# Optimization experiments

Measured on AMD Instinct MI355X. Metric: run time of the kernel, lower is better.

The kernel has to match this reference:

```python
import jax, jax.numpy as jnp
import numpy as np

B, S, D, H = 4, 2048, 1024, 16
DK = D // H

def setup_inputs() -> dict:
    key = jax.random.key(0)
    ks = jax.random.split(key, 5)
    x = jax.random.normal(ks[0], (B, S, D), dtype=jnp.float32)
    scale = 1.0 / np.sqrt(D)
    Wq = jax.random.normal(ks[1], (D, D), dtype=jnp.float32) * scale
    Wk = jax.random.normal(ks[2], (D, D), dtype=jnp.float32) * scale
    Wv = jax.random.normal(ks[3], (D, D), dtype=jnp.float32) * scale
    Wo = jax.random.normal(ks[4], (D, D), dtype=jnp.float32) * scale
    return {"x": x, "Wq": Wq, "Wk": Wk, "Wv": Wv, "Wo": Wo}

def reference(x, Wq, Wk, Wv, Wo):
    # F.linear: y = x @ W.T  (weights stored torch-style [out, in])
    q = jnp.einsum('bsd,ed->bse', x, Wq).reshape(B, S, H, DK).transpose(0, 2, 1, 3)
    k = jnp.einsum('bsd,ed->bse', x, Wk).reshape(B, S, H, DK).transpose(0, 2, 1, 3)
    v = jnp.einsum('bsd,ed->bse', x, Wv).reshape(B, S, H, DK).transpose(0, 2, 1, 3)
    scores = jnp.einsum('bhqd,bhkd->bhqk', q, k) / jnp.sqrt(jnp.float32(DK))
    attn = jax.nn.softmax(scores, axis=-1)  # dropout p=0.0 -> identity
    out = jnp.einsum('bhqk,bhkd->bhqd', attn, v)
    out = out.transpose(0, 2, 1, 3).reshape(B, S, D)
    return jnp.einsum('bsd,ed->bse', out, Wo)
```

## Files before the change

kernel.cpp:

```cpp
#include <hip/hip_runtime.h>
#include <hip/hip_bf16.h>

#define B_ 4
#define S_ 2048
#define D_ 1024
#define H_ 16
#define DK_ 64

typedef __attribute__((ext_vector_type(8))) short short8;
typedef __attribute__((ext_vector_type(4))) float floatx4;
typedef __attribute__((ext_vector_type(16))) float floatx16;
typedef __attribute__((ext_vector_type(4))) unsigned int uint4v;

#define QSCL 0.1803368801111204f

static __device__ __forceinline__ unsigned short f2bf(float f) {
    unsigned int u = __float_as_uint(f);
    u += 0x7fffu + ((u >> 16) & 1u);
    return (unsigned short)(u >> 16);
}

static __device__ __forceinline__ unsigned int pack2bf_perm(float a, float b) {
    unsigned int u0 = __float_as_uint(a) + 0x8000u;
    unsigned int u1 = __float_as_uint(b) + 0x8000u;
    return __builtin_amdgcn_perm(u1, u0, 0x07060302u);
}

static __device__ __forceinline__ unsigned int pack2bf(float a, float b) {
    return (unsigned int)f2bf(a) | ((unsigned int)f2bf(b) << 16);
}

#define PLSWAP(a, b) asm volatile("v_permlane32_swap_b32 %0, %1" : "+v"(a), "+v"(b))

struct CastAll {
    const float* x;
    const float* w[4];
    unsigned short* xd;
    unsigned short* wd[4];
};

__global__ void cast_all_kernel(CastAll a) {
    int i = blockIdx.x * blockDim.x + threadIdx.x;
    const float* s;
    unsigned short* d;
    int j;
    if (i < 2097152) {
        s = a.x; d = a.xd; j = i;
    } else {
        int k = i - 2097152;
        int w = k >> 18;
        j = k & 262143;
        s = a.w[w]; d = a.wd[w];
    }
    float4 v = ((const float4*)s)[j];
    ushort4 o;
    o.x = f2bf(v.x); o.y = f2bf(v.y); o.z = f2bf(v.z); o.w = f2bf(v.w);
    ((ushort4*)d)[j] = o;
}

template <typename OutT, bool VT2>
__global__ __launch_bounds__(256) void gemm_bt(
    const unsigned short* __restrict__ A,
    const unsigned short* __restrict__ W0,
    const unsigned short* __restrict__ W1,
    const unsigned short* __restrict__ W2,
    OutT* __restrict__ C0, OutT* __restrict__ C1, OutT* __restrict__ C2,
    int M, int N, int K)
{
    __shared__ __align__(16) unsigned short At[128 * 64];
    __shared__ __align__(16) unsigned short Bt[128 * 64];

    const unsigned short* W = (blockIdx.z == 0) ? W0 : ((blockIdx.z == 1) ? W1 : W2);
    OutT* C = (blockIdx.z == 0) ? C0 : ((blockIdx.z == 1) ? C1 : C2);

    const int n0 = blockIdx.x * 128;
    const int m0 = blockIdx.y * 128;
    const int wv = threadIdx.x >> 6;
    const int ln = threadIdx.x & 63;
    const int l31 = ln & 31;
    const int half = ln >> 5;
    const int wm = (wv >> 1) * 64;
    const int wn = (wv & 1) * 64;

    floatx16 acc[2][2];
#pragma unroll
    for (int mt = 0; mt < 2; mt++)
#pragma unroll
        for (int nt = 0; nt < 2; nt++)
#pragma unroll
            for (int e = 0; e < 16; e++) acc[mt][nt][e] = 0.f;

    const int lr = ln >> 3;
    const int lc = (((ln & 7) ^ lr) * 8);
    const int sw = (l31 & 7);

    for (int k0 = 0; k0 < K; k0 += 64) {
        __syncthreads();
#pragma unroll
        for (int c = 0; c < 4; c++) {
            int rowA = wv * 32 + c * 8;
            const unsigned short* gA = A + (size_t)(m0 + rowA + lr) * K + k0 + lc;
            __builtin_amdgcn_global_load_lds(
                (const __attribute__((address_space(1))) void*)gA,
                (__attribute__((address_space(3))) void*)&At[rowA * 64], 16, 0, 0);
            const unsigned short* gB = W + (size_t)(n0 + rowA + lr) * K + k0 + lc;
            __builtin_amdgcn_global_load_lds(
                (const __attribute__((address_space(1))) void*)gB,
                (__attribute__((address_space(3))) void*)&Bt[rowA * 64], 16, 0, 0);
        }
        __syncthreads();

#pragma unroll
        for (int ks = 0; ks < 4; ks++) {
            const int slot = ((ks * 2 + half) ^ sw) * 8;
            short8 af[2], bf[2];
#pragma unroll
            for (int mt = 0; mt < 2; mt++)
                af[mt] = *(const short8*)&At[(wm + mt * 32 + l31) * 64 + slot];
#pragma unroll
            for (int nt = 0; nt < 2; nt++)
                bf[nt] = *(const short8*)&Bt[(wn + nt * 32 + l31) * 64 + slot];
#pragma unroll
            for (int mt = 0; mt < 2; mt++)
#pragma unroll
                for (int nt = 0; nt < 2; nt++)
                    acc[mt][nt] = __builtin_amdgcn_mfma_f32_32x32x16_bf16(af[mt], bf[nt], acc[mt][nt], 0, 0, 0);
        }
    }

    const float esc = (VT2 && blockIdx.z == 0) ? QSCL : 1.0f;

    if constexpr (VT2) {
        if (blockIdx.z == 2) {
            unsigned short* Vt = (unsigned short*)C;
#pragma unroll
            for (int mt = 0; mt < 2; mt++)
#pragma unroll
                for (int nt = 0; nt < 2; nt++)
#pragma unroll
                    for (int rg = 0; rg < 4; rg++) {
                        int col = n0 + wn + nt * 32 + l31;
                        int row0 = m0 + wm + mt * 32 + 4 * half + 8 * rg;
                        int bb = row0 >> 11, ss = row0 & 2047;
                        size_t addr = ((size_t)(bb * 1024 + col)) * 2048 + ss;
                        uint2 pk;
                        pk.x = pack2bf(acc[mt][nt][4 * rg + 0], acc[mt][nt][4 * rg + 1]);
                        pk.y = pack2bf(acc[mt][nt][4 * rg + 2], acc[mt][nt][4 * rg + 3]);
                        *(uint2*)(Vt + addr) = pk;
                    }
            return;
        }
    }

#pragma unroll
    for (int mt = 0; mt < 2; mt++)
#pragma unroll
        for (int nt = 0; nt < 2; nt++)
#pragma unroll
            for (int rg = 0; rg < 4; rg++)
#pragma unroll
                for (int r = 0; r < 4; r++) {
                    int row = m0 + wm + mt * 32 + 4 * half + 8 * rg + r;
                    int col = n0 + wn + nt * 32 + l31;
                    float v = acc[mt][nt][4 * rg + r] * esc;
                    if constexpr (sizeof(OutT) == 2)
                        C[(size_t)row * N + col] = (OutT)f2bf(v);
                    else
                        C[(size_t)row * N + col] = v;
                }
}

__global__ __launch_bounds__(256, 4) void flash_attn(
    const unsigned short* __restrict__ Q,
    const unsigned short* __restrict__ K,
    const unsigned short* __restrict__ Vt,
    unsigned short* __restrict__ O)
{
    __shared__ __align__(16) unsigned short Kt[64 * 72];
    __shared__ __align__(16) unsigned short VT[64 * 72];

    const int qt = blockIdx.x;
    const int h = blockIdx.y;
    const int b = blockIdx.z;
    const int tid = threadIdx.x;
    const int wv = tid >> 6;
    const int ln = tid & 63;
    const int l31 = ln & 31;
    const int half = ln >> 5;

    const size_t base = ((size_t)b * S_) * D_ + (size_t)h * DK_;
    const size_t vtbase = ((size_t)(b * 1024 + h * 64)) * (size_t)S_;

    const int qrow = qt * 128 + wv * 32 + l31;
    short8 qf[4];
    {
        const unsigned short* qp = Q + base + (size_t)qrow * D_ + half * 8;
#pragma unroll
        for (int ks = 0; ks < 4; ks++) qf[ks] = *(const short8*)(qp + ks * 16);
    }

    short8 ones;
#pragma unroll
    for (int e = 0; e < 8; e++) ones[e] = (short)0x3F80;

    floatx16 Oacc[2], lacc;
#pragma unroll
    for (int mt = 0; mt < 2; mt++)
#pragma unroll
        for (int e = 0; e < 16; e++) Oacc[mt][e] = 0.f;
#pragma unroll
    for (int e = 0; e < 16; e++) lacc[e] = 0.f;

    const int srow = tid >> 3;
    const int scol = (tid & 7) * 8;

    for (int kt = 0; kt < S_ / 64; kt++) {
        __syncthreads();
#pragma unroll
        for (int c = 0; c < 2; c++) {
            int row = srow + c * 32;
            *(short8*)&Kt[row * 72 + scol] =
                *(const short8*)(K + base + (size_t)(kt * 64 + row) * D_ + scol);
            *(short8*)&VT[row * 72 + scol] =
                *(const short8*)(Vt + vtbase + (size_t)row * S_ + kt * 64 + scol);
        }
        __syncthreads();

        floatx16 sac[2];
#pragma unroll
        for (int mt = 0; mt < 2; mt++) {
#pragma unroll
            for (int e = 0; e < 16; e++) sac[mt][e] = 0.f;
#pragma unroll
            for (int ks = 0; ks < 4; ks++) {
                short8 kf = *(const short8*)&Kt[(mt * 32 + l31) * 72 + ks * 16 + half * 8];
                sac[mt] = __builtin_amdgcn_mfma_f32_32x32x16_bf16(kf, qf[ks], sac[mt], 0, 0, 0);
            }
        }

        uint2 run[2][4];
#pragma unroll
        for (int mt = 0; mt < 2; mt++)
#pragma unroll
            for (int g = 0; g < 4; g++) {
                float p0 = __builtin_amdgcn_exp2f(sac[mt][4 * g + 0]);
                float p1 = __builtin_amdgcn_exp2f(sac[mt][4 * g + 1]);
                float p2 = __builtin_amdgcn_exp2f(sac[mt][4 * g + 2]);
                float p3 = __builtin_amdgcn_exp2f(sac[mt][4 * g + 3]);
                run[mt][g].x = pack2bf_perm(p0, p1);
                run[mt][g].y = pack2bf_perm(p2, p3);
            }

#pragma unroll
        for (int mt = 0; mt < 2; mt++)
#pragma unroll
            for (int t = 0; t < 2; t++) {
                PLSWAP(run[mt][2 * t].x, run[mt][2 * t + 1].x);
                PLSWAP(run[mt][2 * t].y, run[mt][2 * t + 1].y);
            }

#pragma unroll
        for (int mt2 = 0; mt2 < 2; mt2++)
#pragma unroll
            for (int t = 0; t < 2; t++) {
                int ks = mt2 * 2 + t;
                uint4v u = {run[mt2][2 * t].x, run[mt2][2 * t].y,
                            run[mt2][2 * t + 1].x, run[mt2][2 * t + 1].y};
                short8 pf = __builtin_bit_cast(short8, u);
#pragma unroll
                for (int mt = 0; mt < 2; mt++) {
                    short8 vf = *(const short8*)&VT[(mt * 32 + l31) * 72 + ks * 16 + half * 8];
                    Oacc[mt] = __builtin_amdgcn_mfma_f32_32x32x16_bf16(vf, pf, Oacc[mt], 0, 0, 0);
                }
                lacc = __builtin_amdgcn_mfma_f32_32x32x16_bf16(ones, pf, lacc, 0, 0, 0);
            }
    }

    float inv = 1.0f / lacc[0];

#pragma unroll
    for (int mt = 0; mt < 2; mt++)
#pragma unroll
        for (int g = 0; g < 4; g++) {
            uint2 pk;
            pk.x = pack2bf(Oacc[mt][4 * g + 0] * inv, Oacc[mt][4 * g + 1] * inv);
            pk.y = pack2bf(Oacc[mt][4 * g + 2] * inv, Oacc[mt][4 * g + 3] * inv);
            *(uint2*)(O + base + (size_t)qrow * D_ + mt * 32 + 8 * g + 4 * half) = pk;
        }
}

extern "C" void kernel_launch(void* const* d_in, const int* in_sizes, int n_in,
                              void* d_out, int out_size, void* d_ws, size_t ws_size,
                              hipStream_t stream) {
    const float* x  = (const float*)d_in[0];
    const float* Wq = (const float*)d_in[1];
    const float* Wk = (const float*)d_in[2];
    const float* Wv = (const float*)d_in[3];
    const float* Wo = (const float*)d_in[4];
    float* out = (float*)d_out;

    char* ws = (char*)d_ws;
    const size_t MB = 1024 * 1024;
    unsigned short* xb  = (unsigned short*)(ws);
    unsigned short* wqb = (unsigned short*)(ws + 16 * MB);
    unsigned short* wkb = (unsigned short*)(ws + 18 * MB);
    unsigned short* wvb = (unsigned short*)(ws + 20 * MB);
    unsigned short* wob = (unsigned short*)(ws + 22 * MB);
    unsigned short* Qb  = (unsigned short*)(ws + 24 * MB);
    unsigned short* Kb  = (unsigned short*)(ws + 40 * MB);
    unsigned short* Vtb = (unsigned short*)(ws + 56 * MB);
    unsigned short* Ob  = (unsigned short*)(ws);

    CastAll ca;
    ca.x = x; ca.xd = xb;
    ca.w[0] = Wq; ca.w[1] = Wk; ca.w[2] = Wv; ca.w[3] = Wo;
    ca.wd[0] = wqb; ca.wd[1] = wkb; ca.wd[2] = wvb; ca.wd[3] = wob;
    cast_all_kernel<<<12288, 256, 0, stream>>>(ca);

    dim3 gq(D_ / 128, (B_ * S_) / 128, 3);
    gemm_bt<unsigned short, true><<<gq, 256, 0, stream>>>(
        xb, wqb, wkb, wvb, Qb, Kb, Vtb, B_ * S_, D_, D_);

    dim3 gf(S_ / 128, H_, B_);
    flash_attn<<<gf, 256, 0, stream>>>(Qb, Kb, Vtb, Ob);

    dim3 go(D_ / 128, (B_ * S_) / 128, 1);
    gemm_bt<float, false><<<go, 256, 0, stream>>>(
        Ob, wob, wob, wob, out, out, out, B_ * S_, D_, D_);
}
```

Baseline: 287.4 us.

## Process two query subtiles per wave in flash attention to reuse K/V tiles

Each wave now handles 64 query rows (two 32-row subtiles) instead of 32, so each block covers 256 queries and every K/V tile staged in shared memory feeds twice the MFMA work. The row-sum MFMA against a ones vector is replaced by scalar accumulation of the exp values plus a cross-half shuffle at the end. Pointer increments replace the per-iteration address recomputation. The grid is halved and launch bounds are lowered to 2 blocks per CU to fit the doubled accumulator registers, at the cost of fewer blocks and less occupancy.

```diff
diff --git a/kernel.cpp b/kernel.cpp
--- a/kernel.cpp
+++ b/kernel.cpp
@@ -170,7 +170,7 @@
                 }
 }
 
-__global__ __launch_bounds__(256, 4) void flash_attn(
+__global__ __launch_bounds__(256, 2) void flash_attn(
     const unsigned short* __restrict__ Q,
     const unsigned short* __restrict__ K,
     const unsigned short* __restrict__ Vt,
@@ -191,102 +191,116 @@
     const size_t base = ((size_t)b * S_) * D_ + (size_t)h * DK_;
     const size_t vtbase = ((size_t)(b * 1024 + h * 64)) * (size_t)S_;
 
-    const int qrow = qt * 128 + wv * 32 + l31;
-    short8 qf[4];
-    {
-        const unsigned short* qp = Q + base + (size_t)qrow * D_ + half * 8;
-#pragma unroll
-        for (int ks = 0; ks < 4; ks++) qf[ks] = *(const short8*)(qp + ks * 16);
-    }
-
-    short8 ones;
-#pragma unroll
-    for (int e = 0; e < 8; e++) ones[e] = (short)0x3F80;
-
-    floatx16 Oacc[2], lacc;
-#pragma unroll
-    for (int mt = 0; mt < 2; mt++)
-#pragma unroll
-        for (int e = 0; e < 16; e++) Oacc[mt][e] = 0.f;
-#pragma unroll
-    for (int e = 0; e < 16; e++) lacc[e] = 0.f;
+    const int qrow0 = qt * 256 + wv * 64 + l31;
+    short8 qf[2][4];
+#pragma unroll
+    for (int qh = 0; qh < 2; qh++) {
+        const unsigned short* qp = Q + base + (size_t)(qrow0 + qh * 32) * D_ + half * 8;
+#pragma unroll
+        for (int ks = 0; ks < 4; ks++) qf[qh][ks] = *(const short8*)(qp + ks * 16);
+    }
+
+    floatx16 Oacc[2][2];
+#pragma unroll
+    for (int qh = 0; qh < 2; qh++)
+#pragma unroll
+        for (int mt = 0; mt < 2; mt++)
+#pragma unroll
+            for (int e = 0; e < 16; e++) Oacc[qh][mt][e] = 0.f;
+    float l_i[2] = {0.f, 0.f};
 
     const int srow = tid >> 3;
     const int scol = (tid & 7) * 8;
+    const unsigned short* kp0 = K + base + (size_t)srow * D_ + scol;
+    const unsigned short* kp1 = kp0 + (size_t)32 * D_;
+    const unsigned short* vp0 = Vt + vtbase + (size_t)srow * S_ + scol;
+    const unsigned short* vp1 = vp0 + (size_t)32 * S_;
 
     for (int kt = 0; kt < S_ / 64; kt++) {
         __syncthreads();
-#pragma unroll
-        for (int c = 0; c < 2; c++) {
-            int row = srow + c * 32;
-            *(short8*)&Kt[row * 72 + scol] =
-                *(const short8*)(K + base + (size_t)(kt * 64 + row) * D_ + scol);
-            *(short8*)&VT[row * 72 + scol] =
-                *(const short8*)(Vt + vtbase + (size_t)row * S_ + kt * 64 + scol);
-        }
+        *(short8*)&Kt[srow * 72 + scol] = *(const short8*)kp0;
+        *(short8*)&Kt[(srow + 32) * 72 + scol] = *(const short8*)kp1;
+        *(short8*)&VT[srow * 72 + scol] = *(const short8*)vp0;
+        *(short8*)&VT[(srow + 32) * 72 + scol] = *(const short8*)vp1;
+        kp0 += (size_t)64 * D_; kp1 += (size_t)64 * D_;
+        vp0 += 64; vp1 += 64;
         __syncthreads();
 
-        floatx16 sac[2];
+        uint2 run[2][2][4];
+
 #pragma unroll
         for (int mt = 0; mt < 2; mt++) {
-#pragma unroll
-            for (int e = 0; e < 16; e++) sac[mt][e] = 0.f;
+            floatx16 sac[2];
+#pragma unroll
+            for (int qh = 0; qh < 2; qh++)
+#pragma unroll
+                for (int e = 0; e < 16; e++) sac[qh][e] = 0.f;
 #pragma unroll
             for (int ks = 0; ks < 4; ks++) {
                 short8 kf = *(const short8*)&Kt[(mt * 32 + l31) * 72 + ks * 16 + half * 8];
-                sac[mt] = __builtin_amdgcn_mfma_f32_32x32x16_bf16(kf, qf[ks], sac[mt], 0, 0, 0);
+                sac[0] = __builtin_amdgcn_mfma_f32_32x32x16_bf16(kf, qf[0][ks], sac[0], 0, 0, 0);
+                sac[1] = __builtin_amdgcn_mfma_f32_32x32x16_bf16(kf, qf[1][ks], sac[1], 0, 0, 0);
             }
+#pragma unroll
+            for (int qh = 0; qh < 2; qh++)
+#pragma unroll
+                for (int g = 0; g < 4; g++) {
+                    float p0 = __builtin_amdgcn_exp2f(sac[qh][4 * g + 0]);
+                    float p1 = __builtin_amdgcn_exp2f(sac[qh][4 * g + 1]);
+                    float p2 = __builtin_amdgcn_exp2f(sac[qh][4 * g + 2]);
+                    float p3 = __builtin_amdgcn_exp2f(sac[qh][4 * g + 3]);
+                    l_i[qh] += (p0 + p1) + (p2 + p3);
+                    run[qh][mt][g].x = pack2bf_perm(p0, p1);
+                    run[qh][mt][g].y = pack2bf_perm(p2, p3);
+                }
         }
 
-        uint2 run[2][4];
-#pragma unroll
-        for (int mt = 0; mt < 2; mt++)
-#pragma unroll
-            for (int g = 0; g < 4; g++) {
-                float p0 = __builtin_amdgcn_exp2f(sac[mt][4 * g + 0]);
-                float p1 = __builtin_amdgcn_exp2f(sac[mt][4 * g + 1]);
-                float p2 = __builtin_amdgcn_exp2f(sac[mt][4 * g + 2]);
-                float p3 = __builtin_amdgcn_exp2f(sac[mt][4 * g + 3]);
-                run[mt][g].x = pack2bf_perm(p0, p1);
-                run[mt][g].y = pack2bf_perm(p2, p3);
-            }
-
-#pragma unroll
-        for (int mt = 0; mt < 2; mt++)
-#pragma unroll
-            for (int t = 0; t < 2; t++) {
-                PLSWAP(run[mt][2 * t].x, run[mt][2 * t + 1].x);
-                PLSWAP(run[mt][2 * t].y, run[mt][2 * t + 1].y);
-            }
+#pragma unroll
+        for (int qh = 0; qh < 2; qh++)
+#pragma unroll
+            for (int mt = 0; mt < 2; mt++)
+#pragma unroll
+                for (int t = 0; t < 2; t++) {
+                    PLSWAP(run[qh][mt][2 * t].x, run[qh][mt][2 * t + 1].x);
+                    PLSWAP(run[qh][mt][2 * t].y, run[qh][mt][2 * t + 1].y);
+                }
 
 #pragma unroll
         for (int mt2 = 0; mt2 < 2; mt2++)
 #pragma unroll
             for (int t = 0; t < 2; t++) {
                 int ks = mt2 * 2 + t;
-                uint4v u = {run[mt2][2 * t].x, run[mt2][2 * t].y,
-                            run[mt2][2 * t + 1].x, run[mt2][2 * t + 1].y};
-                short8 pf = __builtin_bit_cast(short8, u);
+                short8 pf[2];
+#pragma unroll
+                for (int qh = 0; qh < 2; qh++) {
+                    uint4v u = {run[qh][mt2][2 * t].x, run[qh][mt2][2 * t].y,
+                                run[qh][mt2][2 * t + 1].x, run[qh][mt2][2 * t + 1].y};
+                    pf[qh] = __builtin_bit_cast(short8, u);
+                }
 #pragma unroll
                 for (int mt = 0; mt < 2; mt++) {
                     short8 vf = *(const short8*)&VT[(mt * 32 + l31) * 72 + ks * 16 + half * 8];
-                    Oacc[mt] = __builtin_amdgcn_mfma_f32_32x32x16_bf16(vf, pf, Oacc[mt], 0, 0, 0);
-                }
-                lacc = __builtin_amdgcn_mfma_f32_32x32x16_bf16(ones, pf, lacc, 0, 0, 0);
+                    Oacc[0][mt] = __builtin_amdgcn_mfma_f32_32x32x16_bf16(vf, pf[0], Oacc[0][mt], 0, 0, 0);
+                    Oacc[1][mt] = __builtin_amdgcn_mfma_f32_32x32x16_bf16(vf, pf[1], Oacc[1][mt], 0, 0, 0);
+                }
             }
     }
 
-    float inv = 1.0f / lacc[0];
-
-#pragma unroll
-    for (int mt = 0; mt < 2; mt++)
-#pragma unroll
-        for (int g = 0; g < 4; g++) {
-            uint2 pk;
-            pk.x = pack2bf(Oacc[mt][4 * g + 0] * inv, Oacc[mt][4 * g + 1] * inv);
-            pk.y = pack2bf(Oacc[mt][4 * g + 2] * inv, Oacc[mt][4 * g + 3] * inv);
-            *(uint2*)(O + base + (size_t)qrow * D_ + mt * 32 + 8 * g + 4 * half) = pk;
-        }
+#pragma unroll
+    for (int qh = 0; qh < 2; qh++) {
+        float ls = l_i[qh] + __shfl_xor(l_i[qh], 32);
+        float inv = 1.0f / ls;
+        const size_t orow = base + (size_t)(qrow0 + qh * 32) * D_;
+#pragma unroll
+        for (int mt = 0; mt < 2; mt++)
+#pragma unroll
+            for (int g = 0; g < 4; g++) {
+                uint2 pk;
+                pk.x = pack2bf(Oacc[qh][mt][4 * g + 0] * inv, Oacc[qh][mt][4 * g + 1] * inv);
+                pk.y = pack2bf(Oacc[qh][mt][4 * g + 2] * inv, Oacc[qh][mt][4 * g + 3] * inv);
+                *(uint2*)(O + orow + mt * 32 + 8 * g + 4 * half) = pk;
+            }
+    }
 }
 
 extern "C" void kernel_launch(void* const* d_in, const int* in_sizes, int n_in,
@@ -321,7 +335,7 @@
     gemm_bt<unsigned short, true><<<gq, 256, 0, stream>>>(
         xb, wqb, wkb, wvb, Qb, Kb, Vtb, B_ * S_, D_, D_);
 
-    dim3 gf(S_ / 128, H_, B_);
+    dim3 gf(S_ / 256, H_, B_);
     flash_attn<<<gf, 256, 0, stream>>>(Qb, Kb, Vtb, Ob);
 
     dim3 go(D_ / 128, (B_ * S_) / 128, 1);
```

Result: no change. 282.0 us (-1.9%).

## Load K/V tiles via global_load_lds with XOR-swizzled unpadded LDS layout

Applied to the files above, without the earlier changes.

Replaces the register-staged global-to-LDS copy of K and V^T tiles with direct global_load_lds (buffer-to-LDS) transfers. The padded 72-wide LDS rows become 64-wide with an XOR swizzle of the 16-byte chunks, so bank conflicts stay low without padding. Probability packing also drops round-to-nearest and simply truncates fp32 to bf16, saving adds but adding a small bias to P. The aim is to cut VGPR traffic and instruction count in the inner loop. The load is still synchronous, with barriers around it.

```diff
diff --git a/kernel.cpp b/kernel.cpp
--- a/kernel.cpp
+++ b/kernel.cpp
@@ -20,10 +20,8 @@
     return (unsigned short)(u >> 16);
 }
 
-static __device__ __forceinline__ unsigned int pack2bf_perm(float a, float b) {
-    unsigned int u0 = __float_as_uint(a) + 0x8000u;
-    unsigned int u1 = __float_as_uint(b) + 0x8000u;
-    return __builtin_amdgcn_perm(u1, u0, 0x07060302u);
+static __device__ __forceinline__ unsigned int pack2bf_trunc(float a, float b) {
+    return __builtin_amdgcn_perm(__float_as_uint(b), __float_as_uint(a), 0x07060302u);
 }
 
 static __device__ __forceinline__ unsigned int pack2bf(float a, float b) {
@@ -176,8 +174,8 @@
     const unsigned short* __restrict__ Vt,
     unsigned short* __restrict__ O)
 {
-    __shared__ __align__(16) unsigned short Kt[64 * 72];
-    __shared__ __align__(16) unsigned short VT[64 * 72];
+    __shared__ __align__(16) unsigned short Kt[64 * 64];
+    __shared__ __align__(16) unsigned short VT[64 * 64];
 
     const int qt = blockIdx.x;
     const int h = blockIdx.y;
@@ -211,19 +209,33 @@
 #pragma unroll
     for (int e = 0; e < 16; e++) lacc[e] = 0.f;
 
-    const int srow = tid >> 3;
-    const int scol = (tid & 7) * 8;
+    const int lrow = ln >> 3;
+    const int lchk = (ln & 7) ^ lrow;
+    const unsigned short* kg = K + base + (size_t)(wv * 16 + lrow) * D_ + lchk * 8;
+    const unsigned short* vg = Vt + vtbase + (size_t)(wv * 16 + lrow) * S_ + lchk * 8;
+    unsigned short* ldsK0 = &Kt[(wv * 16) * 64];
+    unsigned short* ldsK1 = &Kt[(wv * 16 + 8) * 64];
+    unsigned short* ldsV0 = &VT[(wv * 16) * 64];
+    unsigned short* ldsV1 = &VT[(wv * 16 + 8) * 64];
+
+    const int sw = (l31 & 7);
 
     for (int kt = 0; kt < S_ / 64; kt++) {
         __syncthreads();
-#pragma unroll
-        for (int c = 0; c < 2; c++) {
-            int row = srow + c * 32;
-            *(short8*)&Kt[row * 72 + scol] =
-                *(const short8*)(K + base + (size_t)(kt * 64 + row) * D_ + scol);
-            *(short8*)&VT[row * 72 + scol] =
-                *(const short8*)(Vt + vtbase + (size_t)row * S_ + kt * 64 + scol);
-        }
+        __builtin_amdgcn_global_load_lds(
+            (const __attribute__((address_space(1))) void*)kg,
+            (__attribute__((address_space(3))) void*)ldsK0, 16, 0, 0);
+        __builtin_amdgcn_global_load_lds(
+            (const __attribute__((address_space(1))) void*)(kg + 8 * D_),
+            (__attribute__((address_space(3))) void*)ldsK1, 16, 0, 0);
+        __builtin_amdgcn_global_load_lds(
+            (const __attribute__((address_space(1))) void*)vg,
+            (__attribute__((address_space(3))) void*)ldsV0, 16, 0, 0);
+        __builtin_amdgcn_global_load_lds(
+            (const __attribute__((address_space(1))) void*)(vg + 8 * S_),
+            (__attribute__((address_space(3))) void*)ldsV1, 16, 0, 0);
+        kg += (size_t)64 * D_;
+        vg += 64;
         __syncthreads();
 
         floatx16 sac[2];
@@ -233,7 +245,8 @@
             for (int e = 0; e < 16; e++) sac[mt][e] = 0.f;
 #pragma unroll
             for (int ks = 0; ks < 4; ks++) {
-                short8 kf = *(const short8*)&Kt[(mt * 32 + l31) * 72 + ks * 16 + half * 8];
+                const int slot = ((ks * 2 + half) ^ sw) * 8;
+                short8 kf = *(const short8*)&Kt[(mt * 32 + l31) * 64 + slot];
                 sac[mt] = __builtin_amdgcn_mfma_f32_32x32x16_bf16(kf, qf[ks], sac[mt], 0, 0, 0);
             }
         }
@@ -247,8 +260,8 @@
                 float p1 = __builtin_amdgcn_exp2f(sac[mt][4 * g + 1]);
                 float p2 = __builtin_amdgcn_exp2f(sac[mt][4 * g + 2]);
                 float p3 = __builtin_amdgcn_exp2f(sac[mt][4 * g + 3]);
-                run[mt][g].x = pack2bf_perm(p0, p1);
-                run[mt][g].y = pack2bf_perm(p2, p3);
+                run[mt][g].x = pack2bf_trunc(p0, p1);
+                run[mt][g].y = pack2bf_trunc(p2, p3);
             }
 
 #pragma unroll
@@ -267,9 +280,10 @@
                 uint4v u = {run[mt2][2 * t].x, run[mt2][2 * t].y,
                             run[mt2][2 * t + 1].x, run[mt2][2 * t + 1].y};
                 short8 pf = __builtin_bit_cast(short8, u);
+                const int slot = ((ks * 2 + half) ^ sw) * 8;
 #pragma unroll
                 for (int mt = 0; mt < 2; mt++) {
-                    short8 vf = *(const short8*)&VT[(mt * 32 + l31) * 72 + ks * 16 + half * 8];
+                    short8 vf = *(const short8*)&VT[(mt * 32 + l31) * 64 + slot];
                     Oacc[mt] = __builtin_amdgcn_mfma_f32_32x32x16_bf16(vf, pf, Oacc[mt], 0, 0, 0);
                 }
                 lacc = __builtin_amdgcn_mfma_f32_32x32x16_bf16(ones, pf, lacc, 0, 0, 0);
```

After: 291.5 us. About the same (+1.4%).
